# Optimization experiments

Hardware: AMD Instinct MI355X
Metric: run time of the kernel (lower is better)

The kernel has to match this reference:

```python
import jax, jax.numpy as jnp
import numpy as np

B, N, O, C, D = 1, 256, 12, 128, 32  # batch, points, orientations, num_hidden, basis_dim


def setup_inputs() -> dict:
    key = jax.random.key(0)
    k0, k1, k2, k3, k4, k5 = jax.random.split(key, 6)
    return {
        "x": jax.random.normal(k0, (B, N, O, C), dtype=jnp.float32),
        "kernel_basis": jax.random.normal(k1, (B, N, N, O, D), dtype=jnp.float32),
        "fiber_kernel_basis": jax.random.normal(k2, (O, O, D), dtype=jnp.float32),
        "mask": jnp.ones((B, N), dtype=jnp.float32),
        "W_spatial": jax.random.normal(k3, (D, C), dtype=jnp.float32) / np.sqrt(D),
        "W_rot": jax.random.normal(k4, (D, C), dtype=jnp.float32) / np.sqrt(D),
        "bias": jnp.zeros((C,), dtype=jnp.float32),
    }


def reference(x, kernel_basis, fiber_kernel_basis, mask, W_spatial, W_rot, bias):
    # Dense (no bias) projections of the bases: last dim D -> C
    spatial_kernel = jnp.einsum("bmnod,dc->bmnoc", kernel_basis, W_spatial)  # (B,M,N,O,C)
    rot_kernel = jnp.einsum("pod,dc->poc", fiber_kernel_basis, W_rot)        # (O,O,C)
    # spatial aggregation over source points n (mask-weighted)
    y = jnp.einsum("bnoc,bmnoc,bn->bmoc", x, spatial_kernel, mask)           # (B,M,O,C)
    # fiber (orientation) rotation, averaged over o
    y = jnp.einsum("bmoc,poc->bmpc", y, rot_kernel) / rot_kernel.shape[-2]   # (B,M,O,C)
    return y + bias
```

## Files before the change

kernel.cpp:

```cpp
#include <hip/hip_runtime.h>
#include <hip/hip_bf16.h>

#define N_ 256
#define M_ 256
#define O_ 12
#define C_ 128
#define D_ 32
#define S2 16
#define KBROW 393216

typedef __attribute__((ext_vector_type(8))) short short8;
typedef __attribute__((ext_vector_type(4))) float floatx4;

#define GLD16(GSRC, LDST) \
    __builtin_amdgcn_global_load_lds( \
        (const __attribute__((address_space(1))) void*)(GSRC), \
        (__attribute__((address_space(3))) void*)(LDST), 16, 0, 0)

static __device__ __forceinline__ short2 pk2(float a, float b) {
    union { __hip_bfloat162 h; short2 s; } u;
    u.h = __float22bfloat162_rn(make_float2(a, b));
    return u.s;
}

__global__ __launch_bounds__(256) void prep2_kernel(
    const float* __restrict__ x, const float* __restrict__ mask,
    const float* __restrict__ fkb, const float* __restrict__ Wr,
    float* __restrict__ xmm, float* __restrict__ rk)
{
    const int b = blockIdx.x;
    const int t = threadIdx.x;
    if (b < 1536) {
        const int idx = b * 256 + t;
        const int n = idx / (O_ * C_);
        xmm[idx] = x[idx] * mask[n];
    } else {
        const int idx = (b - 1536) * 256 + t;
        const int c  = idx & (C_ - 1);
        const int po = idx >> 7;
        const float* f = fkb + po * D_;
        float acc = 0.f;
#pragma unroll
        for (int d = 0; d < D_; ++d) acc = fmaf(f[d], Wr[d * C_ + c], acc);
        rk[idx] = acc;
    }
}

__global__ __launch_bounds__(768, 3) void spatial6_kernel(
    const float* __restrict__ kb, const float* __restrict__ xmm,
    const float* __restrict__ Ws, float* __restrict__ part)
{
    const int mt  = blockIdx.x;
    const int sck = blockIdx.y;
    const int t = threadIdx.x;
    const int lane = t & 63;
    const int w = t >> 6;
    const int l15 = lane & 15;
    const int lk  = lane >> 4;
    const int m0 = mt * 16;
    const int n0 = sck * 16;

    __shared__ __align__(16) char Abuf[4 * 24576];

    const int j0 = w * 128 + lane;
    const int j1 = j0 + 64;
    const int r0 = j0 / 96, s0j = j0 % 96;
    const int r1 = j1 / 96, s1j = j1 % 96;
    const char* kbc = (const char*)kb;
    const char* src0 = kbc + (size_t)(m0 + r0) * KBROW + (size_t)n0 * 1536
                       + (size_t)((s0j ^ (r0 & 7)) * 16);
    const char* src1 = kbc + (size_t)(m0 + r1) * KBROW + (size_t)n0 * 1536
                       + (size_t)((s1j ^ (r1 & 7)) * 16);
    char* dst0 = Abuf + w * 2048;
    char* dst1 = Abuf + w * 2048 + 1024;

#define STAGE(BIX, S) { \
    GLD16(src0 + (size_t)(S) * 1536, dst0 + (BIX) * 24576); \
    GLD16(src1 + (size_t)(S) * 1536, dst1 + (BIX) * 24576); }

    float wsr[8][8];
#pragma unroll
    for (int cg = 0; cg < 8; ++cg)
#pragma unroll
        for (int i = 0; i < 8; ++i)
            wsr[cg][i] = Ws[(lk * 8 + i) * C_ + cg * 16 + l15];

    const int off0 = l15 * 1536 + (((w * 8 + lk * 2    ) ^ (l15 & 7)) * 16);
    const int off1 = l15 * 1536 + (((w * 8 + lk * 2 + 1) ^ (l15 & 7)) * 16);

    const float* xb = xmm + ((size_t)n0 * O_ + w) * C_ + l15;

    floatx4 acc[8];
#pragma unroll
    for (int cg = 0; cg < 8; ++cg)
#pragma unroll
        for (int q = 0; q < 4; ++q) acc[cg][q] = 0.f;

    STAGE(0, 0);
    STAGE(1, 1);

    float xvA[8], xvB[8];
#pragma unroll
    for (int cg = 0; cg < 8; ++cg) xvA[cg] = xb[cg * 16];

#define PHASE(S, BIX, XC, XN) { \
    asm volatile("s_waitcnt vmcnt(10)" ::: "memory"); \
    __builtin_amdgcn_s_barrier(); \
    if ((S) + 2 < 16) STAGE(((BIX) + 2) & 3, (S) + 2); \
    const char* ab_ = Abuf + (BIX) * 24576; \
    const floatx4 a0_ = *(const floatx4*)(ab_ + off0); \
    const floatx4 a1_ = *(const floatx4*)(ab_ + off1); \
    union { short8 v; short2 p2[4]; } au_; \
    au_.p2[0] = pk2(a0_[0], a0_[1]); au_.p2[1] = pk2(a0_[2], a0_[3]); \
    au_.p2[2] = pk2(a1_[0], a1_[1]); au_.p2[3] = pk2(a1_[2], a1_[3]); \
    _Pragma("unroll") \
    for (int cg = 0; cg < 8; ++cg) { \
        union { short8 v; short2 p2[4]; } bu_; \
        bu_.p2[0] = pk2(XC[cg] * wsr[cg][0], XC[cg] * wsr[cg][1]); \
        bu_.p2[1] = pk2(XC[cg] * wsr[cg][2], XC[cg] * wsr[cg][3]); \
        bu_.p2[2] = pk2(XC[cg] * wsr[cg][4], XC[cg] * wsr[cg][5]); \
        bu_.p2[3] = pk2(XC[cg] * wsr[cg][6], XC[cg] * wsr[cg][7]); \
        acc[cg] = __builtin_amdgcn_mfma_f32_16x16x32_bf16(au_.v, bu_.v, acc[cg], 0, 0, 0); \
    } \
    if ((S) + 1 < 16) { \
        _Pragma("unroll") \
        for (int cg = 0; cg < 8; ++cg) \
            XN[cg] = xb[(size_t)((S) + 1) * (O_ * C_) + cg * 16]; \
    } }

    for (int sb = 0; sb < 16; sb += 4) {
        PHASE(sb + 0, 0, xvA, xvB)
        PHASE(sb + 1, 1, xvB, xvA)
        PHASE(sb + 2, 2, xvA, xvB)
        PHASE(sb + 3, 3, xvB, xvA)
    }
#undef PHASE
#undef STAGE

#pragma unroll
    for (int cg = 0; cg < 8; ++cg) {
        const int c = cg * 16 + l15;
#pragma unroll
        for (int j = 0; j < 4; ++j) {
            const int m = m0 + lk * 4 + j;
            part[(((size_t)m * S2 + sck) * O_ + w) * C_ + c] = acc[cg][j];
        }
    }
}

__global__ __launch_bounds__(256) void fiber3_kernel(
    const float* __restrict__ part, const float* __restrict__ rkv,
    const float* __restrict__ bias, float* __restrict__ out)
{
    const int m = blockIdx.x;
    const int t = threadIdx.x;
    const int c = t & 127;
    const int half = t >> 7;
    float y1v[O_];
#pragma unroll
    for (int o = 0; o < O_; ++o) {
        float a = 0.f;
#pragma unroll
        for (int s = 0; s < S2; ++s)
            a += part[(((size_t)m * S2 + s) * O_ + o) * C_ + c];
        y1v[o] = a;
    }
#pragma unroll
    for (int pp = 0; pp < O_ / 2; ++pp) {
        const int p = half * (O_ / 2) + pp;
        float a = 0.f;
#pragma unroll
        for (int o = 0; o < O_; ++o)
            a = fmaf(y1v[o], rkv[(p * O_ + o) * C_ + c], a);
        out[((size_t)m * O_ + p) * C_ + c] = a * (1.f / 12.f) + bias[c];
    }
}

__global__ __launch_bounds__(256) void spatial_old_kernel(
    const float* __restrict__ x, const float* __restrict__ kb,
    const float* __restrict__ mask, const float* __restrict__ Ws,
    float* __restrict__ y1)
{
    const int bid = blockIdx.x;
    const int m = bid / O_, o = bid % O_;
    const int tid = threadIdx.x;
    const int h = tid >> 7, c = tid & (C_ - 1);
    __shared__ float kbs[2][8][D_];
    __shared__ float msk[N_];
    __shared__ float Ts[2][D_][C_];
    msk[tid] = mask[tid];
    float T[D_];
#pragma unroll
    for (int d = 0; d < D_; ++d) T[d] = 0.f;
    const float* kb_mo = kb + (size_t)m * (N_ * O_ * D_) + o * D_;
    const int j_ld = c >> 4, d_ld = (c & 15) * 2;
    for (int chunk = 0; chunk < 16; ++chunk) {
        const int n0 = h * 128 + chunk * 8;
        __syncthreads();
        float2 v = *reinterpret_cast<const float2*>(
            kb_mo + (size_t)(n0 + j_ld) * (O_ * D_) + d_ld);
        kbs[h][j_ld][d_ld] = v.x;
        kbs[h][j_ld][d_ld + 1] = v.y;
        __syncthreads();
#pragma unroll
        for (int j = 0; j < 8; ++j) {
            const int n = n0 + j;
            const float xv = x[(n * O_ + o) * C_ + c] * msk[n];
#pragma unroll
            for (int d = 0; d < D_; ++d) T[d] = fmaf(kbs[h][j][d], xv, T[d]);
        }
    }
#pragma unroll
    for (int d = 0; d < D_; ++d) Ts[h][d][c] = T[d];
    __syncthreads();
    if (h == 0) {
        float a = 0.f;
#pragma unroll
        for (int d = 0; d < D_; ++d)
            a = fmaf(Ts[0][d][c] + Ts[1][d][c], Ws[d * C_ + c], a);
        y1[((size_t)m * O_ + o) * C_ + c] = a;
    }
}

__global__ __launch_bounds__(256) void fiber_old_kernel(
    const float* __restrict__ y1, const float* __restrict__ rkv,
    const float* __restrict__ bias, float* __restrict__ out)
{
    int idx = blockIdx.x * 256 + threadIdx.x;
    if (idx >= M_ * O_ * C_) return;
    int c = idx & (C_ - 1);
    int p = (idx >> 7) % O_;
    int m = idx / (O_ * C_);
    float a = 0.f;
#pragma unroll
    for (int o = 0; o < O_; ++o)
        a = fmaf(y1[(m * O_ + o) * C_ + c], rkv[(p * O_ + o) * C_ + c], a);
    out[idx] = a * (1.0f / 12.0f) + bias[c];
}

__global__ __launch_bounds__(256) void rot_proj_kernel(
    const float* __restrict__ fkb, const float* __restrict__ Wr,
    float* __restrict__ rk)
{
    int idx = blockIdx.x * 256 + threadIdx.x;
    if (idx >= O_ * O_ * C_) return;
    int c  = idx & (C_ - 1);
    int po = idx >> 7;
    const float* f = fkb + po * D_;
    float acc = 0.f;
#pragma unroll
    for (int d = 0; d < D_; ++d) acc = fmaf(f[d], Wr[d * C_ + c], acc);
    rk[idx] = acc;
}

extern "C" void kernel_launch(void* const* d_in, const int* in_sizes, int n_in,
                              void* d_out, int out_size, void* d_ws, size_t ws_size,
                              hipStream_t stream)
{
    const float* x    = (const float*)d_in[0];
    const float* kb   = (const float*)d_in[1];
    const float* fkb  = (const float*)d_in[2];
    const float* mask = (const float*)d_in[3];
    const float* Wsp  = (const float*)d_in[4];
    const float* Wrt  = (const float*)d_in[5];
    const float* bias = (const float*)d_in[6];
    float* out = (float*)d_out;

    const size_t RK_F   = (size_t)O_ * O_ * C_;
    const size_t PART_F = (size_t)M_ * S2 * O_ * C_;
    const size_t XMM_F  = (size_t)N_ * O_ * C_;
    const size_t need   = (RK_F + PART_F + XMM_F) * 4;

    float* rk = (float*)d_ws;

    if (ws_size >= need) {
        float* part = rk + RK_F;
        float* xmm  = part + PART_F;
        prep2_kernel<<<1536 + (O_ * O_ * C_) / 256, 256, 0, stream>>>(
            x, mask, fkb, Wrt, xmm, rk);
        spatial6_kernel<<<dim3(16, 16), 768, 0, stream>>>(kb, xmm, Wsp, part);
        fiber3_kernel<<<M_, 256, 0, stream>>>(part, rk, bias, out);
    } else {
        float* y1 = rk + RK_F;
        rot_proj_kernel<<<(O_ * O_ * C_ + 255) / 256, 256, 0, stream>>>(fkb, Wrt, rk);
        spatial_old_kernel<<<M_ * O_, 256, 0, stream>>>(x, kb, mask, Wsp, y1);
        fiber_old_kernel<<<(M_ * O_ * C_ + 255) / 256, 256, 0, stream>>>(y1, rk, bias, out);
    }
}
```

Before: 43.22 us.

## Fuse prep into spatial kernel and store partial sums as bf16

Removes the separate prep kernel. The mask multiply now happens inside the spatial MFMA loop using a small shared-memory mask table, and the rotation-kernel projection is computed by block (0,0) at the end of the spatial kernel. The per-split partial sums are written as bf16 instead of fp32, halving the intermediate buffer written by the spatial kernel and read by the fiber kernel. The fiber kernel is rewritten to reduce the bf16 partials with vector loads into shared memory before the orientation contraction. Risks are extra rounding error from the bf16 partials and a longer tail on the one block that also does the rotation projection.

```diff
diff --git a/kernel.cpp b/kernel.cpp
--- a/kernel.cpp
+++ b/kernel.cpp
@@ -23,32 +23,21 @@
     return u.s;
 }
 
-__global__ __launch_bounds__(256) void prep2_kernel(
-    const float* __restrict__ x, const float* __restrict__ mask,
+static __device__ __forceinline__ short f2bf(float f) {
+    unsigned u = __float_as_uint(f);
+    unsigned r = u + 0x7FFFu + ((u >> 16) & 1u);
+    return (short)(r >> 16);
+}
+
+static __device__ __forceinline__ float bf2f(short s) {
+    return __uint_as_float(((unsigned)(unsigned short)s) << 16);
+}
+
+__global__ __launch_bounds__(768, 3) void spatial6b_kernel(
+    const float* __restrict__ kb, const float* __restrict__ x,
+    const float* __restrict__ mask, const float* __restrict__ Ws,
     const float* __restrict__ fkb, const float* __restrict__ Wr,
-    float* __restrict__ xmm, float* __restrict__ rk)
-{
-    const int b = blockIdx.x;
-    const int t = threadIdx.x;
-    if (b < 1536) {
-        const int idx = b * 256 + t;
-        const int n = idx / (O_ * C_);
-        xmm[idx] = x[idx] * mask[n];
-    } else {
-        const int idx = (b - 1536) * 256 + t;
-        const int c  = idx & (C_ - 1);
-        const int po = idx >> 7;
-        const float* f = fkb + po * D_;
-        float acc = 0.f;
-#pragma unroll
-        for (int d = 0; d < D_; ++d) acc = fmaf(f[d], Wr[d * C_ + c], acc);
-        rk[idx] = acc;
-    }
-}
-
-__global__ __launch_bounds__(768, 3) void spatial6_kernel(
-    const float* __restrict__ kb, const float* __restrict__ xmm,
-    const float* __restrict__ Ws, float* __restrict__ part)
+    short* __restrict__ part16, float* __restrict__ rk)
 {
     const int mt  = blockIdx.x;
     const int sck = blockIdx.y;
@@ -61,6 +50,10 @@
     const int n0 = sck * 16;
 
     __shared__ __align__(16) char Abuf[4 * 24576];
+    __shared__ float mskL[16];
+
+    if (t < 16) mskL[t] = mask[n0 + t];
+    asm volatile("s_waitcnt lgkmcnt(0)" ::: "memory");
 
     const int j0 = w * 128 + lane;
     const int j1 = j0 + 64;
@@ -88,7 +81,7 @@
     const int off0 = l15 * 1536 + (((w * 8 + lk * 2    ) ^ (l15 & 7)) * 16);
     const int off1 = l15 * 1536 + (((w * 8 + lk * 2 + 1) ^ (l15 & 7)) * 16);
 
-    const float* xb = xmm + ((size_t)n0 * O_ + w) * C_ + l15;
+    const float* xb = x + ((size_t)n0 * O_ + w) * C_ + l15;
 
     floatx4 acc[8];
 #pragma unroll
@@ -107,6 +100,7 @@
     asm volatile("s_waitcnt vmcnt(10)" ::: "memory"); \
     __builtin_amdgcn_s_barrier(); \
     if ((S) + 2 < 16) STAGE(((BIX) + 2) & 3, (S) + 2); \
+    const float mk_ = mskL[S]; \
     const char* ab_ = Abuf + (BIX) * 24576; \
     const floatx4 a0_ = *(const floatx4*)(ab_ + off0); \
     const floatx4 a1_ = *(const floatx4*)(ab_ + off1); \
@@ -115,11 +109,12 @@
     au_.p2[2] = pk2(a1_[0], a1_[1]); au_.p2[3] = pk2(a1_[2], a1_[3]); \
     _Pragma("unroll") \
     for (int cg = 0; cg < 8; ++cg) { \
+        const float xm_ = XC[cg] * mk_; \
         union { short8 v; short2 p2[4]; } bu_; \
-        bu_.p2[0] = pk2(XC[cg] * wsr[cg][0], XC[cg] * wsr[cg][1]); \
-        bu_.p2[1] = pk2(XC[cg] * wsr[cg][2], XC[cg] * wsr[cg][3]); \
-        bu_.p2[2] = pk2(XC[cg] * wsr[cg][4], XC[cg] * wsr[cg][5]); \
-        bu_.p2[3] = pk2(XC[cg] * wsr[cg][6], XC[cg] * wsr[cg][7]); \
+        bu_.p2[0] = pk2(xm_ * wsr[cg][0], xm_ * wsr[cg][1]); \
+        bu_.p2[1] = pk2(xm_ * wsr[cg][2], xm_ * wsr[cg][3]); \
+        bu_.p2[2] = pk2(xm_ * wsr[cg][4], xm_ * wsr[cg][5]); \
+        bu_.p2[3] = pk2(xm_ * wsr[cg][6], xm_ * wsr[cg][7]); \
         acc[cg] = __builtin_amdgcn_mfma_f32_16x16x32_bf16(au_.v, bu_.v, acc[cg], 0, 0, 0); \
     } \
     if ((S) + 1 < 16) { \
@@ -143,35 +138,58 @@
 #pragma unroll
         for (int j = 0; j < 4; ++j) {
             const int m = m0 + lk * 4 + j;
-            part[(((size_t)m * S2 + sck) * O_ + w) * C_ + c] = acc[cg][j];
+            part16[(((size_t)m * S2 + sck) * O_ + w) * C_ + c] = f2bf(acc[cg][j]);
         }
     }
-}
-
-__global__ __launch_bounds__(256) void fiber3_kernel(
-    const float* __restrict__ part, const float* __restrict__ rkv,
+
+    if (mt == 0 && sck == 0) {
+#pragma unroll 2
+        for (int i = t; i < O_ * O_ * C_; i += 768) {
+            const int c  = i & (C_ - 1);
+            const int po = i >> 7;
+            const float* f = fkb + po * D_;
+            float a = 0.f;
+#pragma unroll
+            for (int d = 0; d < D_; ++d) a = fmaf(f[d], Wr[d * C_ + c], a);
+            rk[i] = a;
+        }
+    }
+}
+
+__global__ __launch_bounds__(256) void fiber4_kernel(
+    const short* __restrict__ part16, const float* __restrict__ rkv,
     const float* __restrict__ bias, float* __restrict__ out)
 {
     const int m = blockIdx.x;
     const int t = threadIdx.x;
-    const int c = t & 127;
-    const int half = t >> 7;
-    float y1v[O_];
-#pragma unroll
-    for (int o = 0; o < O_; ++o) {
+    __shared__ float y1L[O_][C_];
+
+    if (t < 192) {
+        const int o  = t >> 4;
+        const int c0 = (t & 15) * 8;
+        float a[8];
+#pragma unroll
+        for (int i = 0; i < 8; ++i) a[i] = 0.f;
+#pragma unroll
+        for (int s = 0; s < S2; ++s) {
+            const short8 v = *reinterpret_cast<const short8*>(
+                part16 + (((size_t)m * S2 + s) * O_ + o) * C_ + c0);
+#pragma unroll
+            for (int i = 0; i < 8; ++i) a[i] += bf2f(v[i]);
+        }
+#pragma unroll
+        for (int i = 0; i < 8; ++i) y1L[o][c0 + i] = a[i];
+    }
+    __syncthreads();
+
+#pragma unroll
+    for (int k = t; k < O_ * C_; k += 256) {
+        const int p = k >> 7;
+        const int c = k & (C_ - 1);
         float a = 0.f;
 #pragma unroll
-        for (int s = 0; s < S2; ++s)
-            a += part[(((size_t)m * S2 + s) * O_ + o) * C_ + c];
-        y1v[o] = a;
-    }
-#pragma unroll
-    for (int pp = 0; pp < O_ / 2; ++pp) {
-        const int p = half * (O_ / 2) + pp;
-        float a = 0.f;
-#pragma unroll
         for (int o = 0; o < O_; ++o)
-            a = fmaf(y1v[o], rkv[(p * O_ + o) * C_ + c], a);
+            a = fmaf(y1L[o][c], rkv[(p * O_ + o) * C_ + c], a);
         out[((size_t)m * O_ + p) * C_ + c] = a * (1.f / 12.f) + bias[c];
     }
 }
@@ -266,20 +284,17 @@
     const float* bias = (const float*)d_in[6];
     float* out = (float*)d_out;
 
-    const size_t RK_F   = (size_t)O_ * O_ * C_;
-    const size_t PART_F = (size_t)M_ * S2 * O_ * C_;
-    const size_t XMM_F  = (size_t)N_ * O_ * C_;
-    const size_t need   = (RK_F + PART_F + XMM_F) * 4;
+    const size_t RK_F    = (size_t)O_ * O_ * C_;
+    const size_t PART_E  = (size_t)M_ * S2 * O_ * C_;
+    const size_t need    = RK_F * 4 + PART_E * 2;
 
     float* rk = (float*)d_ws;
 
     if (ws_size >= need) {
-        float* part = rk + RK_F;
-        float* xmm  = part + PART_F;
-        prep2_kernel<<<1536 + (O_ * O_ * C_) / 256, 256, 0, stream>>>(
-            x, mask, fkb, Wrt, xmm, rk);
-        spatial6_kernel<<<dim3(16, 16), 768, 0, stream>>>(kb, xmm, Wsp, part);
-        fiber3_kernel<<<M_, 256, 0, stream>>>(part, rk, bias, out);
+        short* part16 = (short*)(rk + RK_F);
+        spatial6b_kernel<<<dim3(16, 16), 768, 0, stream>>>(
+            kb, x, mask, Wsp, fkb, Wrt, part16, rk);
+        fiber4_kernel<<<M_, 256, 0, stream>>>(part16, rk, bias, out);
     } else {
         float* y1 = rk + RK_F;
         rot_proj_kernel<<<(O_ * O_ * C_ + 255) / 256, 256, 0, stream>>>(fkb, Wrt, rk);
```

New measurement: 53.75 us. 1.24x slower.
